# Kernel optimization log

Hardware: AMD Instinct MI355X
Metric: run time of the kernel (lower is better)

## Reference

```python
import jax, jax.numpy as jnp
import numpy as np

B, D, ADA, INTER, RANK = 16, 2048, 1024, 1024, 8

def setup_inputs() -> dict:
    key = jax.random.key(0)
    ks = jax.random.split(key, 7)
    s = lambda fan_in: 1.0 / np.sqrt(fan_in)
    return {
        "x": jax.random.normal(ks[0], (B, D), jnp.float32),
        "ada_emb": jax.random.normal(ks[1], (B, ADA), jnp.float32),
        "base": jax.random.normal(ks[2], (D, D), jnp.float32),  # nn.Parameter(torch.randn)
        "w1": jax.random.normal(ks[3], (ADA, INTER), jnp.float32) * s(ADA),
        "b1": jax.random.normal(ks[4], (INTER,), jnp.float32) * s(ADA),
        "w2": jax.random.normal(ks[5], (INTER, D * RANK * 2), jnp.float32) * s(INTER),
        "b2": jax.random.normal(ks[6], (D * RANK * 2,), jnp.float32) * s(INTER),
    }

def reference(x, ada_emb, base, w1, b1, w2, b2):
    Bn, Dn = x.shape
    # gen_weight: Linear -> GELU (exact, erf-based as torch nn.GELU) -> Linear
    h = jax.nn.gelu(ada_emb @ w1 + b1, approximate=False)
    xw = h @ w2 + b2                               # [B, D*rank*2]
    x_a, x_b = jnp.split(xw, 2, axis=-1)
    r = x_a.shape[-1] // Dn
    x_a = x_a.reshape(Bn, Dn, r)                   # [B, D, r]
    x_b = x_b.reshape(Bn, Dn, r)                   # [B, D, r]
    # per-sample low-rank delta + base: layer[b,d,k] = base[d,k] + sum_r x_a[b,d,r]*x_b[b,k,r]
    layer = base[None, :, :] + jnp.einsum('bdr,bkr->bdk', x_a, x_b)  # [B, D, D]
    out = jnp.einsum('bc,bco->bo', x, layer)       # batched matvec
    return x + out                                 # residual
```

## Files before the change

kernel.cpp:

```cpp
#include <hip/hip_runtime.h>
#include <math.h>

#define BN 16
#define DN 2048
#define ADA 1024
#define INTER 1024
#define NW2 32768
#define HALFN 16384
#define KSL 16

typedef __attribute__((address_space(1))) const void gv_t;
typedef __attribute__((address_space(3))) void lv_t;
__device__ __forceinline__ void gload_lds16(const float* g, float* l) {
    __builtin_amdgcn_global_load_lds((gv_t*)g, (lv_t*)l, 16, 0, 0);
}

__global__ void k1a(const float* __restrict__ ada, const float* __restrict__ w1,
                    float* __restrict__ h_pre) {
    const int j  = blockIdx.x * 256 + threadIdx.x;
    const int k0 = blockIdx.y * 32;
    __shared__ float a_lds[BN][32];
    for (int idx = threadIdx.x; idx < BN * 32; idx += 256) {
        int m = idx >> 5, kk = idx & 31;
        a_lds[m][kk] = ada[m * ADA + k0 + kk];
    }
    __syncthreads();
    float acc[BN];
#pragma unroll
    for (int m = 0; m < BN; ++m) acc[m] = 0.f;
    for (int kk = 0; kk < 32; ++kk) {
        float w = w1[(k0 + kk) * INTER + j];
#pragma unroll
        for (int m = 0; m < BN; ++m) acc[m] += a_lds[m][kk] * w;
    }
#pragma unroll
    for (int m = 0; m < BN; ++m) atomicAdd(&h_pre[m * INTER + j], acc[m]);
}

__global__ void k1bt(const float* __restrict__ h_pre, const float* __restrict__ b1,
                     float* __restrict__ h_t) {
    int i = blockIdx.x * 256 + threadIdx.x;
    int m = i >> 10, j = i & (INTER - 1);
    float v = h_pre[i] + b1[j];
    float g = 0.5f * v * (1.f + erff(v * 0.70710678118654752f));
    h_t[j * BN + m] = g;
}

__global__ __launch_bounds__(256) void k2g(const float* __restrict__ h_t,
                                           const float* __restrict__ w2,
                                           float* __restrict__ p2) {
    const int tid = threadIdx.x;
    const int wv_ = tid >> 6, ln_ = tid & 63;
    const int n0  = blockIdx.x * 1024;
    const int k0  = blockIdx.y * 64;
    __shared__ __align__(16) float wl[2][8][1024];
    __shared__ __align__(16) float hl[64][16];

    ((float4*)hl)[tid] = ((const float4*)(h_t + k0 * BN))[tid];

    float4 acc[BN];
#pragma unroll
    for (int m = 0; m < BN; ++m) acc[m] = make_float4(0.f, 0.f, 0.f, 0.f);

#define STAGE(buf, ph) do {                                                   \
    const float* gs_ = w2 + (size_t)(k0 + (ph) * 8) * NW2 + n0                \
                     + wv_ * 256 + ln_ * 4;                                   \
    float* ls_ = &wl[buf][0][wv_ * 256];                                      \
    _Pragma("unroll")                                                         \
    for (int i_ = 0; i_ < 8; ++i_)                                            \
        gload_lds16(gs_ + (size_t)i_ * NW2, ls_ + i_ * 1024);                 \
} while (0)

#define COMPUTE(buf, ph) do {                                                 \
    _Pragma("unroll")                                                         \
    for (int i_ = 0; i_ < 8; ++i_) {                                          \
        const int kk_ = (ph) * 8 + i_;                                        \
        const float4 wvv = ((const float4*)wl[buf][i_])[tid];                 \
        const float4 h0 = ((const float4*)&hl[kk_][0])[0];                    \
        const float4 h1 = ((const float4*)&hl[kk_][0])[1];                    \
        const float4 h2 = ((const float4*)&hl[kk_][0])[2];                    \
        const float4 h3 = ((const float4*)&hl[kk_][0])[3];                    \
        AC(0,  h0.x); AC(1,  h0.y); AC(2,  h0.z); AC(3,  h0.w);               \
        AC(4,  h1.x); AC(5,  h1.y); AC(6,  h1.z); AC(7,  h1.w);               \
        AC(8,  h2.x); AC(9,  h2.y); AC(10, h2.z); AC(11, h2.w);               \
        AC(12, h3.x); AC(13, h3.y); AC(14, h3.z); AC(15, h3.w);               \
    }                                                                         \
} while (0)
#define AC(m, hs) do { acc[m].x = fmaf(hs, wvv.x, acc[m].x);                  \
                       acc[m].y = fmaf(hs, wvv.y, acc[m].y);                  \
                       acc[m].z = fmaf(hs, wvv.z, acc[m].z);                  \
                       acc[m].w = fmaf(hs, wvv.w, acc[m].w); } while (0)

    STAGE(0, 0);
    __syncthreads();
    for (int ph = 0; ph < 8; ++ph) {
        const int cur = ph & 1;
        if (ph < 7) STAGE(cur ^ 1, ph + 1);
        COMPUTE(cur, ph);
        __syncthreads();
    }
#undef AC
#undef COMPUTE
#undef STAGE

    float* op = p2 + (size_t)blockIdx.y * (BN * NW2) + n0 + tid * 4;
#pragma unroll
    for (int m = 0; m < BN; ++m)
        *(float4*)(op + (size_t)m * NW2) = acc[m];
}

__global__ void k2r(const float* __restrict__ p2, const float* __restrict__ b2,
                    float* __restrict__ xw) {
    const int i  = blockIdx.x * 256 + threadIdx.x;
    const int n4 = i & (NW2 / 4 - 1);
    float4 s = ((const float4*)b2)[n4];
    const float4* p = (const float4*)p2 + i;
#pragma unroll
    for (int ks = 0; ks < KSL; ++ks) {
        float4 v = p[(size_t)ks * (BN * NW2 / 4)];
        s.x += v.x; s.y += v.y; s.z += v.z; s.w += v.w;
    }
    ((float4*)xw)[i] = s;
}

__global__ void k3(const float* __restrict__ x, const float* __restrict__ xw,
                   float* __restrict__ t) {
    const int m = blockIdx.x >> 3, r = blockIdx.x & 7;
    float s = 0.f;
    for (int c = threadIdx.x; c < DN; c += 256)
        s += x[m * DN + c] * xw[(size_t)m * NW2 + c * 8 + r];
    __shared__ float red[256];
    red[threadIdx.x] = s;
    __syncthreads();
    for (int off = 128; off > 0; off >>= 1) {
        if (threadIdx.x < off) red[threadIdx.x] += red[threadIdx.x + off];
        __syncthreads();
    }
    if (threadIdx.x == 0) t[m * 8 + r] = red[0];
}

#define K4ACC(i, xv) do { acc[i].x = fmaf((xv), b.x, acc[i].x); \
                          acc[i].y = fmaf((xv), b.y, acc[i].y); \
                          acc[i].z = fmaf((xv), b.z, acc[i].z); \
                          acc[i].w = fmaf((xv), b.w, acc[i].w); } while (0)
__global__ __launch_bounds__(256) void k4m(const float* __restrict__ x,
                                           const float* __restrict__ base,
                                           float* __restrict__ p4) {
    const int o4 = blockIdx.x * 256 + threadIdx.x;
    const int c0 = blockIdx.y * 32;
    const int m0 = blockIdx.z * 8;
    float4 acc[8];
#pragma unroll
    for (int m = 0; m < 8; ++m) acc[m] = make_float4(0.f, 0.f, 0.f, 0.f);

    const float4* bp = (const float4*)base + (size_t)c0 * (DN / 4) + o4;
    float4 bbuf[8];
#pragma unroll
    for (int u = 0; u < 8; ++u) bbuf[u] = bp[(size_t)u * (DN / 4)];

    for (int cb = 0; cb < 32; cb += 8) {
#pragma unroll
        for (int u = 0; u < 8; ++u) {
            const int cc = cb + u;
            const float4 b = bbuf[u];
            const int cn = (cc + 8 < 32) ? (cc + 8) : cc;
            bbuf[u] = bp[(size_t)cn * (DN / 4)];
            const float x0 = x[(m0 + 0) * DN + c0 + cc];
            const float x1 = x[(m0 + 1) * DN + c0 + cc];
            const float x2 = x[(m0 + 2) * DN + c0 + cc];
            const float x3 = x[(m0 + 3) * DN + c0 + cc];
            const float x4 = x[(m0 + 4) * DN + c0 + cc];
            const float x5 = x[(m0 + 5) * DN + c0 + cc];
            const float x6 = x[(m0 + 6) * DN + c0 + cc];
            const float x7 = x[(m0 + 7) * DN + c0 + cc];
            K4ACC(0, x0); K4ACC(1, x1); K4ACC(2, x2); K4ACC(3, x3);
            K4ACC(4, x4); K4ACC(5, x5); K4ACC(6, x6); K4ACC(7, x7);
        }
    }
    float4* op = (float4*)p4 + (size_t)blockIdx.y * (BN * DN / 4)
               + (size_t)m0 * (DN / 4) + o4;
#pragma unroll
    for (int m = 0; m < 8; ++m) op[(size_t)m * (DN / 4)] = acc[m];
}

__global__ void k5(const float* __restrict__ x, const float* __restrict__ p4,
                   const float* __restrict__ xw, const float* __restrict__ t,
                   float* __restrict__ out) {
    const int i = blockIdx.x * 256 + threadIdx.x;
    const int m = i >> 11, o = i & (DN - 1);
    float s = x[i];
    const float* p = p4 + i;
#pragma unroll 8
    for (int ks = 0; ks < 64; ++ks) s += p[ks * (BN * DN)];
    const float4 xb0 = *(const float4*)(xw + (size_t)m * NW2 + HALFN + o * 8);
    const float4 xb1 = *(const float4*)(xw + (size_t)m * NW2 + HALFN + o * 8 + 4);
    const float* tm = t + m * 8;
    s += tm[0] * xb0.x + tm[1] * xb0.y + tm[2] * xb0.z + tm[3] * xb0.w
       + tm[4] * xb1.x + tm[5] * xb1.y + tm[6] * xb1.z + tm[7] * xb1.w;
    out[i] = s;
}

extern "C" void kernel_launch(void* const* d_in, const int* in_sizes, int n_in,
                              void* d_out, int out_size, void* d_ws, size_t ws_size,
                              hipStream_t stream) {
    const float* x    = (const float*)d_in[0];
    const float* ada  = (const float*)d_in[1];
    const float* base = (const float*)d_in[2];
    const float* w1   = (const float*)d_in[3];
    const float* b1   = (const float*)d_in[4];
    const float* w2   = (const float*)d_in[5];
    const float* b2   = (const float*)d_in[6];
    float* out = (float*)d_out;
    char* ws = (char*)d_ws;

    float* p2    = (float*)(ws);
    float* xw    = (float*)(ws + 33554432);
    float* p4    = (float*)(ws + 35651584);
    float* h_pre = (float*)(ws + 44040192);
    float* h_t   = (float*)(ws + 44105728);
    float* t     = (float*)(ws + 44171264);

    hipMemsetAsync(h_pre, 0, 65536, stream);

    k1a <<<dim3(4, 32),    256, 0, stream>>>(ada, w1, h_pre);
    k1bt<<<64,             256, 0, stream>>>(h_pre, b1, h_t);
    k2g <<<dim3(32, KSL),  256, 0, stream>>>(h_t, w2, p2);
    k4m <<<dim3(2, 64, 2), 256, 0, stream>>>(x, base, p4);
    k2r <<<512,            256, 0, stream>>>(p2, b2, xw);
    k3  <<<128,            256, 0, stream>>>(x, xw, t);
    k5  <<<128,            256, 0, stream>>>(x, p4, xw, t, out);
}
```

Baseline: 82.32 us.

## Merge w2 GEMM and base matvec into one launch with triple-buffered LDS pipeline

Fuses the w2 split-K GEMM and the base matvec into a single kernel that picks its role from the block index, so the two memory-bound streams run concurrently. The w2 path moves to 4-row stages, triple buffering and explicit vmcnt waits with raw barriers. The first GEMM drops the memset and atomics in favour of split-K partials reduced in the GELU kernel, and x is staged in LDS for the base path. The cost is more workspace traffic for the partials and an occupancy hint of 3 blocks per CU that may limit registers.

```diff
diff --git a/kernel.cpp b/kernel.cpp
--- a/kernel.cpp
+++ b/kernel.cpp
@@ -14,16 +14,16 @@
 __device__ __forceinline__ void gload_lds16(const float* g, float* l) {
     __builtin_amdgcn_global_load_lds((gv_t*)g, (lv_t*)l, 16, 0, 0);
 }
+#define WAITV(N) asm volatile("s_waitcnt vmcnt(" #N ")" ::: "memory")
+#define WAITL0() asm volatile("s_waitcnt lgkmcnt(0)" ::: "memory")
 
 __global__ void k1a(const float* __restrict__ ada, const float* __restrict__ w1,
-                    float* __restrict__ h_pre) {
+                    float* __restrict__ p1) {
     const int j  = blockIdx.x * 256 + threadIdx.x;
     const int k0 = blockIdx.y * 32;
-    __shared__ float a_lds[BN][32];
-    for (int idx = threadIdx.x; idx < BN * 32; idx += 256) {
-        int m = idx >> 5, kk = idx & 31;
-        a_lds[m][kk] = ada[m * ADA + k0 + kk];
-    }
+    __shared__ float al[32][16];
+    for (int i = threadIdx.x; i < 512; i += 256)
+        al[i >> 4][i & 15] = ada[(i & 15) * ADA + k0 + (i >> 4)];
     __syncthreads();
     float acc[BN];
 #pragma unroll
@@ -31,82 +31,149 @@
     for (int kk = 0; kk < 32; ++kk) {
         float w = w1[(k0 + kk) * INTER + j];
 #pragma unroll
-        for (int m = 0; m < BN; ++m) acc[m] += a_lds[m][kk] * w;
-    }
-#pragma unroll
-    for (int m = 0; m < BN; ++m) atomicAdd(&h_pre[m * INTER + j], acc[m]);
-}
-
-__global__ void k1bt(const float* __restrict__ h_pre, const float* __restrict__ b1,
+        for (int m = 0; m < BN; ++m) acc[m] += al[kk][m] * w;
+    }
+    float* op = p1 + (size_t)blockIdx.y * (BN * INTER) + j;
+#pragma unroll
+    for (int m = 0; m < BN; ++m) op[m * INTER] = acc[m];
+}
+
+__global__ void k1bt(const float* __restrict__ p1, const float* __restrict__ b1,
                      float* __restrict__ h_t) {
     int i = blockIdx.x * 256 + threadIdx.x;
-    int m = i >> 10, j = i & (INTER - 1);
-    float v = h_pre[i] + b1[j];
+    int m = i >> 10, k = i & (INTER - 1);
+    float v = b1[k];
+#pragma unroll 8
+    for (int ks = 0; ks < 32; ++ks) v += p1[ks * (BN * INTER) + i];
     float g = 0.5f * v * (1.f + erff(v * 0.70710678118654752f));
-    h_t[j * BN + m] = g;
-}
-
-__global__ __launch_bounds__(256) void k2g(const float* __restrict__ h_t,
-                                           const float* __restrict__ w2,
-                                           float* __restrict__ p2) {
+    h_t[k * BN + m] = g;
+}
+
+__global__ __launch_bounds__(256, 3) void kbig(const float* __restrict__ h_t,
+                                               const float* __restrict__ w2,
+                                               const float* __restrict__ x,
+                                               const float* __restrict__ base,
+                                               float* __restrict__ p2,
+                                               float* __restrict__ p4) {
+    __shared__ __align__(16) float smem[13312];
     const int tid = threadIdx.x;
-    const int wv_ = tid >> 6, ln_ = tid & 63;
-    const int n0  = blockIdx.x * 1024;
-    const int k0  = blockIdx.y * 64;
-    __shared__ __align__(16) float wl[2][8][1024];
-    __shared__ __align__(16) float hl[64][16];
-
-    ((float4*)hl)[tid] = ((const float4*)(h_t + k0 * BN))[tid];
-
-    float4 acc[BN];
-#pragma unroll
-    for (int m = 0; m < BN; ++m) acc[m] = make_float4(0.f, 0.f, 0.f, 0.f);
-
-#define STAGE(buf, ph) do {                                                   \
-    const float* gs_ = w2 + (size_t)(k0 + (ph) * 8) * NW2 + n0                \
-                     + wv_ * 256 + ln_ * 4;                                   \
-    float* ls_ = &wl[buf][0][wv_ * 256];                                      \
+    const int bx  = blockIdx.x;
+
+    if (bx < 512) {
+        float* wl = smem;
+        float* hl = smem + 12288;
+        const int nt = bx & 31, ks = bx >> 5;
+        const int n0 = nt * 1024, k0 = ks * 64;
+        const int wv = tid >> 6, ln = tid & 63;
+
+        ((float4*)hl)[tid] = ((const float4*)(h_t + k0 * BN))[tid];
+
+        float4 acc[BN];
+#pragma unroll
+        for (int m = 0; m < BN; ++m) acc[m] = make_float4(0.f, 0.f, 0.f, 0.f);
+
+#define STAGE(b, ph) do {                                                     \
+    const float* gs_ = w2 + (size_t)(k0 + (ph) * 4) * NW2 + n0                \
+                     + wv * 256 + ln * 4;                                     \
+    float* ls_ = wl + (b) * 4096 + wv * 256;                                  \
+    gload_lds16(gs_ + (size_t)0 * NW2, ls_ + 0 * 1024);                       \
+    gload_lds16(gs_ + (size_t)1 * NW2, ls_ + 1 * 1024);                       \
+    gload_lds16(gs_ + (size_t)2 * NW2, ls_ + 2 * 1024);                       \
+    gload_lds16(gs_ + (size_t)3 * NW2, ls_ + 3 * 1024);                       \
+} while (0)
+#define AC(m, hs) do { acc[m].x = fmaf(hs, wvv.x, acc[m].x);                  \
+                       acc[m].y = fmaf(hs, wvv.y, acc[m].y);                  \
+                       acc[m].z = fmaf(hs, wvv.z, acc[m].z);                  \
+                       acc[m].w = fmaf(hs, wvv.w, acc[m].w); } while (0)
+#define COMPUTE(b, ph) do {                                                   \
     _Pragma("unroll")                                                         \
-    for (int i_ = 0; i_ < 8; ++i_)                                            \
-        gload_lds16(gs_ + (size_t)i_ * NW2, ls_ + i_ * 1024);                 \
-} while (0)
-
-#define COMPUTE(buf, ph) do {                                                 \
-    _Pragma("unroll")                                                         \
-    for (int i_ = 0; i_ < 8; ++i_) {                                          \
-        const int kk_ = (ph) * 8 + i_;                                        \
-        const float4 wvv = ((const float4*)wl[buf][i_])[tid];                 \
-        const float4 h0 = ((const float4*)&hl[kk_][0])[0];                    \
-        const float4 h1 = ((const float4*)&hl[kk_][0])[1];                    \
-        const float4 h2 = ((const float4*)&hl[kk_][0])[2];                    \
-        const float4 h3 = ((const float4*)&hl[kk_][0])[3];                    \
+    for (int i_ = 0; i_ < 4; ++i_) {                                          \
+        const int kk_ = (ph) * 4 + i_;                                        \
+        const float4 wvv = ((const float4*)(wl + (b) * 4096 + i_ * 1024))[tid];\
+        const float4 h0 = ((const float4*)(hl + kk_ * 16))[0];                \
+        const float4 h1 = ((const float4*)(hl + kk_ * 16))[1];                \
+        const float4 h2 = ((const float4*)(hl + kk_ * 16))[2];                \
+        const float4 h3 = ((const float4*)(hl + kk_ * 16))[3];                \
         AC(0,  h0.x); AC(1,  h0.y); AC(2,  h0.z); AC(3,  h0.w);               \
         AC(4,  h1.x); AC(5,  h1.y); AC(6,  h1.z); AC(7,  h1.w);               \
         AC(8,  h2.x); AC(9,  h2.y); AC(10, h2.z); AC(11, h2.w);               \
         AC(12, h3.x); AC(13, h3.y); AC(14, h3.z); AC(15, h3.w);               \
     }                                                                         \
 } while (0)
-#define AC(m, hs) do { acc[m].x = fmaf(hs, wvv.x, acc[m].x);                  \
-                       acc[m].y = fmaf(hs, wvv.y, acc[m].y);                  \
-                       acc[m].z = fmaf(hs, wvv.z, acc[m].z);                  \
-                       acc[m].w = fmaf(hs, wvv.w, acc[m].w); } while (0)
-
-    STAGE(0, 0);
-    __syncthreads();
-    for (int ph = 0; ph < 8; ++ph) {
-        const int cur = ph & 1;
-        if (ph < 7) STAGE(cur ^ 1, ph + 1);
-        COMPUTE(cur, ph);
+
+        STAGE(0, 0);
+        STAGE(1, 1);
+        WAITL0();
+#pragma unroll
+        for (int ph = 0; ph < 16; ++ph) {
+            if (ph < 15) { WAITV(4); } else { WAITV(0); }
+            __builtin_amdgcn_s_barrier();
+            __builtin_amdgcn_sched_barrier(0);
+            if (ph < 14) {
+                const int nb = (ph + 2) % 3;
+                STAGE(nb, ph + 2);
+            }
+            const int cb = ph % 3;
+            COMPUTE(cb, ph);
+        }
+#undef COMPUTE
+#undef AC
+#undef STAGE
+
+        float* op = p2 + (size_t)ks * (BN * NW2) + n0 + tid * 4;
+#pragma unroll
+        for (int m = 0; m < BN; ++m)
+            *(float4*)(op + (size_t)m * NW2) = acc[m];
+
+    } else {
+        const int id2 = bx - 512;
+        const int o4 = (id2 & 1) * 256 + tid;
+        const int c0 = ((id2 >> 1) & 63) * 32;
+        const int m0 = (id2 >> 7) * 8;
+        float* xl = smem;
+        for (int i = tid; i < 512; i += 256)
+            xl[i] = x[(i & 15) * DN + c0 + (i >> 4)];
         __syncthreads();
-    }
-#undef AC
-#undef COMPUTE
-#undef STAGE
-
-    float* op = p2 + (size_t)blockIdx.y * (BN * NW2) + n0 + tid * 4;
-#pragma unroll
-    for (int m = 0; m < BN; ++m)
-        *(float4*)(op + (size_t)m * NW2) = acc[m];
+
+        float4 acc[8];
+#pragma unroll
+        for (int m = 0; m < 8; ++m) acc[m] = make_float4(0.f, 0.f, 0.f, 0.f);
+
+        const float4* bp = (const float4*)base + (size_t)c0 * (DN / 4) + o4;
+        float4 bbuf[8];
+#pragma unroll
+        for (int u = 0; u < 8; ++u) bbuf[u] = bp[(size_t)u * (DN / 4)];
+
+        for (int cb = 0; cb < 32; cb += 8) {
+#pragma unroll
+            for (int u = 0; u < 8; ++u) {
+                const int cc = cb + u;
+                const float4 b = bbuf[u];
+                const int cn = (cc + 8 < 32) ? (cc + 8) : cc;
+                bbuf[u] = bp[(size_t)cn * (DN / 4)];
+                const float4 x0 = *(const float4*)&xl[cc * 16 + 0];
+                const float4 x1 = *(const float4*)&xl[cc * 16 + 4];
+                const float4 x2 = *(const float4*)&xl[cc * 16 + 8];
+                const float4 x3 = *(const float4*)&xl[cc * 16 + 12];
+#define A4(mm, xs) do { acc[mm].x = fmaf(xs, b.x, acc[mm].x);                 \
+                        acc[mm].y = fmaf(xs, b.y, acc[mm].y);                 \
+                        acc[mm].z = fmaf(xs, b.z, acc[mm].z);                 \
+                        acc[mm].w = fmaf(xs, b.w, acc[mm].w); } while (0)
+                if (m0 == 0) {
+                    A4(0, x0.x); A4(1, x0.y); A4(2, x0.z); A4(3, x0.w);
+                    A4(4, x1.x); A4(5, x1.y); A4(6, x1.z); A4(7, x1.w);
+                } else {
+                    A4(0, x2.x); A4(1, x2.y); A4(2, x2.z); A4(3, x2.w);
+                    A4(4, x3.x); A4(5, x3.y); A4(6, x3.z); A4(7, x3.w);
+                }
+#undef A4
+            }
+        }
+        float4* op = (float4*)p4 + (size_t)((id2 >> 1) & 63) * (BN * DN / 4)
+                   + (size_t)m0 * (DN / 4) + o4;
+#pragma unroll
+        for (int m = 0; m < 8; ++m) op[(size_t)m * (DN / 4)] = acc[m];
+    }
 }
 
 __global__ void k2r(const float* __restrict__ p2, const float* __restrict__ b2,
@@ -137,50 +204,6 @@
         __syncthreads();
     }
     if (threadIdx.x == 0) t[m * 8 + r] = red[0];
-}
-
-#define K4ACC(i, xv) do { acc[i].x = fmaf((xv), b.x, acc[i].x); \
-                          acc[i].y = fmaf((xv), b.y, acc[i].y); \
-                          acc[i].z = fmaf((xv), b.z, acc[i].z); \
-                          acc[i].w = fmaf((xv), b.w, acc[i].w); } while (0)
-__global__ __launch_bounds__(256) void k4m(const float* __restrict__ x,
-                                           const float* __restrict__ base,
-                                           float* __restrict__ p4) {
-    const int o4 = blockIdx.x * 256 + threadIdx.x;
-    const int c0 = blockIdx.y * 32;
-    const int m0 = blockIdx.z * 8;
-    float4 acc[8];
-#pragma unroll
-    for (int m = 0; m < 8; ++m) acc[m] = make_float4(0.f, 0.f, 0.f, 0.f);
-
-    const float4* bp = (const float4*)base + (size_t)c0 * (DN / 4) + o4;
-    float4 bbuf[8];
-#pragma unroll
-    for (int u = 0; u < 8; ++u) bbuf[u] = bp[(size_t)u * (DN / 4)];
-
-    for (int cb = 0; cb < 32; cb += 8) {
-#pragma unroll
-        for (int u = 0; u < 8; ++u) {
-            const int cc = cb + u;
-            const float4 b = bbuf[u];
-            const int cn = (cc + 8 < 32) ? (cc + 8) : cc;
-            bbuf[u] = bp[(size_t)cn * (DN / 4)];
-            const float x0 = x[(m0 + 0) * DN + c0 + cc];
-            const float x1 = x[(m0 + 1) * DN + c0 + cc];
-            const float x2 = x[(m0 + 2) * DN + c0 + cc];
-            const float x3 = x[(m0 + 3) * DN + c0 + cc];
-            const float x4 = x[(m0 + 4) * DN + c0 + cc];
-            const float x5 = x[(m0 + 5) * DN + c0 + cc];
-            const float x6 = x[(m0 + 6) * DN + c0 + cc];
-            const float x7 = x[(m0 + 7) * DN + c0 + cc];
-            K4ACC(0, x0); K4ACC(1, x1); K4ACC(2, x2); K4ACC(3, x3);
-            K4ACC(4, x4); K4ACC(5, x5); K4ACC(6, x6); K4ACC(7, x7);
-        }
-    }
-    float4* op = (float4*)p4 + (size_t)blockIdx.y * (BN * DN / 4)
-               + (size_t)m0 * (DN / 4) + o4;
-#pragma unroll
-    for (int m = 0; m < 8; ++m) op[(size_t)m * (DN / 4)] = acc[m];
 }
 
 __global__ void k5(const float* __restrict__ x, const float* __restrict__ p4,
@@ -213,20 +236,17 @@
     float* out = (float*)d_out;
     char* ws = (char*)d_ws;
 
-    float* p2    = (float*)(ws);
-    float* xw    = (float*)(ws + 33554432);
-    float* p4    = (float*)(ws + 35651584);
-    float* h_pre = (float*)(ws + 44040192);
-    float* h_t   = (float*)(ws + 44105728);
-    float* t     = (float*)(ws + 44171264);
-
-    hipMemsetAsync(h_pre, 0, 65536, stream);
-
-    k1a <<<dim3(4, 32),    256, 0, stream>>>(ada, w1, h_pre);
-    k1bt<<<64,             256, 0, stream>>>(h_pre, b1, h_t);
-    k2g <<<dim3(32, KSL),  256, 0, stream>>>(h_t, w2, p2);
-    k4m <<<dim3(2, 64, 2), 256, 0, stream>>>(x, base, p4);
-    k2r <<<512,            256, 0, stream>>>(p2, b2, xw);
-    k3  <<<128,            256, 0, stream>>>(x, xw, t);
-    k5  <<<128,            256, 0, stream>>>(x, p4, xw, t, out);
-}
+    float* p2  = (float*)(ws);
+    float* p4  = (float*)(ws + 33554432);
+    float* p1  = (float*)(ws + 41943040);
+    float* xw  = (float*)(ws + 44040192);
+    float* h_t = (float*)(ws + 46137344);
+    float* t   = (float*)(ws + 46202880);
+
+    k1a <<<dim3(4, 32), 256, 0, stream>>>(ada, w1, p1);
+    k1bt<<<64,          256, 0, stream>>>(p1, b1, h_t);
+    kbig<<<768,         256, 0, stream>>>(h_t, w2, x, base, p2, p4);
+    k2r <<<512,         256, 0, stream>>>(p2, b2, xw);
+    k3  <<<128,         256, 0, stream>>>(x, xw, t);
+    k5  <<<128,         256, 0, stream>>>(x, p4, xw, t, out);
+}
```

New measurement: 228.7 us. 2.78x slower.

## Triple-buffer w2 staging in k2 GEMM with explicit vmcnt waits

Applied to the files above, without the earlier changes.

Replaces the double-buffered 8-row LDS staging of w2 with a three-stage ring of 4-row buffers, keeping two global->LDS loads in flight. Explicit s_waitcnt vmcnt(4) plus a raw s_barrier replace __syncthreads, so the wait covers only the oldest stage. The aim is to hide more memory latency on the w2 stream, which dominates this kernel. The cost is more barriers per block and correctness that depends on hand-counted outstanding loads.

```diff
diff --git a/kernel.cpp b/kernel.cpp
--- a/kernel.cpp
+++ b/kernel.cpp
@@ -14,6 +14,9 @@
 __device__ __forceinline__ void gload_lds16(const float* g, float* l) {
     __builtin_amdgcn_global_load_lds((gv_t*)g, (lv_t*)l, 16, 0, 0);
 }
+#define WAITV4() asm volatile("s_waitcnt vmcnt(4)" ::: "memory")
+#define WAITV0() asm volatile("s_waitcnt vmcnt(0)" ::: "memory")
+#define WAITL0() asm volatile("s_waitcnt lgkmcnt(0)" ::: "memory")
 
 __global__ void k1a(const float* __restrict__ ada, const float* __restrict__ w1,
                     float* __restrict__ h_pre) {
@@ -46,36 +49,41 @@
     h_t[j * BN + m] = g;
 }
 
-__global__ __launch_bounds__(256) void k2g(const float* __restrict__ h_t,
+__global__ __launch_bounds__(256) void k2p(const float* __restrict__ h_t,
                                            const float* __restrict__ w2,
                                            float* __restrict__ p2) {
     const int tid = threadIdx.x;
-    const int wv_ = tid >> 6, ln_ = tid & 63;
+    const int wv  = tid >> 6, ln = tid & 63;
     const int n0  = blockIdx.x * 1024;
     const int k0  = blockIdx.y * 64;
-    __shared__ __align__(16) float wl[2][8][1024];
+    __shared__ __align__(16) float wl[3][4][1024];
     __shared__ __align__(16) float hl[64][16];
 
     ((float4*)hl)[tid] = ((const float4*)(h_t + k0 * BN))[tid];
+    WAITL0();
 
     float4 acc[BN];
 #pragma unroll
     for (int m = 0; m < BN; ++m) acc[m] = make_float4(0.f, 0.f, 0.f, 0.f);
 
-#define STAGE(buf, ph) do {                                                   \
-    const float* gs_ = w2 + (size_t)(k0 + (ph) * 8) * NW2 + n0                \
-                     + wv_ * 256 + ln_ * 4;                                   \
-    float* ls_ = &wl[buf][0][wv_ * 256];                                      \
+#define STAGE(b, ph) do {                                                     \
+    const float* gs_ = w2 + (size_t)(k0 + (ph) * 4) * NW2 + n0                \
+                     + wv * 256 + ln * 4;                                     \
+    float* ls_ = &wl[b][0][wv * 256];                                         \
+    gload_lds16(gs_ + (size_t)0 * NW2, ls_ + 0 * 1024);                       \
+    gload_lds16(gs_ + (size_t)1 * NW2, ls_ + 1 * 1024);                       \
+    gload_lds16(gs_ + (size_t)2 * NW2, ls_ + 2 * 1024);                       \
+    gload_lds16(gs_ + (size_t)3 * NW2, ls_ + 3 * 1024);                       \
+} while (0)
+#define AC(m, hs) do { acc[m].x = fmaf(hs, wvv.x, acc[m].x);                  \
+                       acc[m].y = fmaf(hs, wvv.y, acc[m].y);                  \
+                       acc[m].z = fmaf(hs, wvv.z, acc[m].z);                  \
+                       acc[m].w = fmaf(hs, wvv.w, acc[m].w); } while (0)
+#define COMPUTE(b, ph) do {                                                   \
     _Pragma("unroll")                                                         \
-    for (int i_ = 0; i_ < 8; ++i_)                                            \
-        gload_lds16(gs_ + (size_t)i_ * NW2, ls_ + i_ * 1024);                 \
-} while (0)
-
-#define COMPUTE(buf, ph) do {                                                 \
-    _Pragma("unroll")                                                         \
-    for (int i_ = 0; i_ < 8; ++i_) {                                          \
-        const int kk_ = (ph) * 8 + i_;                                        \
-        const float4 wvv = ((const float4*)wl[buf][i_])[tid];                 \
+    for (int i_ = 0; i_ < 4; ++i_) {                                          \
+        const int kk_ = (ph) * 4 + i_;                                        \
+        const float4 wvv = ((const float4*)&wl[b][i_][0])[tid];               \
         const float4 h0 = ((const float4*)&hl[kk_][0])[0];                    \
         const float4 h1 = ((const float4*)&hl[kk_][0])[1];                    \
         const float4 h2 = ((const float4*)&hl[kk_][0])[2];                    \
@@ -86,21 +94,23 @@
         AC(12, h3.x); AC(13, h3.y); AC(14, h3.z); AC(15, h3.w);               \
     }                                                                         \
 } while (0)
-#define AC(m, hs) do { acc[m].x = fmaf(hs, wvv.x, acc[m].x);                  \
-                       acc[m].y = fmaf(hs, wvv.y, acc[m].y);                  \
-                       acc[m].z = fmaf(hs, wvv.z, acc[m].z);                  \
-                       acc[m].w = fmaf(hs, wvv.w, acc[m].w); } while (0)
 
     STAGE(0, 0);
-    __syncthreads();
-    for (int ph = 0; ph < 8; ++ph) {
-        const int cur = ph & 1;
-        if (ph < 7) STAGE(cur ^ 1, ph + 1);
-        COMPUTE(cur, ph);
-        __syncthreads();
-    }
+    STAGE(1, 1);
+    int cb = 0, nb = 2;
+    for (int ph = 0; ph < 15; ++ph) {
+        WAITV4();
+        __builtin_amdgcn_s_barrier();
+        if (ph < 14) STAGE(nb, ph + 2);
+        COMPUTE(cb, ph);
+        cb = (cb == 2) ? 0 : cb + 1;
+        nb = (nb == 2) ? 0 : nb + 1;
+    }
+    WAITV0();
+    __builtin_amdgcn_s_barrier();
+    COMPUTE(cb, 15);
+#undef COMPUTE
 #undef AC
-#undef COMPUTE
 #undef STAGE
 
     float* op = p2 + (size_t)blockIdx.y * (BN * NW2) + n0 + tid * 4;
@@ -224,7 +234,7 @@
 
     k1a <<<dim3(4, 32),    256, 0, stream>>>(ada, w1, h_pre);
     k1bt<<<64,             256, 0, stream>>>(h_pre, b1, h_t);
-    k2g <<<dim3(32, KSL),  256, 0, stream>>>(h_t, w2, p2);
+    k2p <<<dim3(32, KSL),  256, 0, stream>>>(h_t, w2, p2);
     k4m <<<dim3(2, 64, 2), 256, 0, stream>>>(x, base, p4);
     k2r <<<512,            256, 0, stream>>>(p2, b2, xw);
     k3  <<<128,            256, 0, stream>>>(x, xw, t);
```

Result: faster. 72.54 us (-11.9%).
